# Kernel tuning notes

Hardware: AMD Instinct MI355X
Metric: run time of the kernel (lower is better)

## Reference

```python
import jax, jax.numpy as jnp
import numpy as np

HD = 64        # hidden_dim
H = 4          # heads
N = 50000      # nodes
E = 400000     # edges (before self loops)
NEG_ATT = 0.2  # GATConv attention LeakyReLU slope (PyG default)
NEG_ACT = 0.01 # nn.LeakyReLU() default slope
EPS = 1e-5     # BatchNorm eps


def _bn(x, gamma, beta):
    # training-mode BatchNorm1d over node dimension (biased variance)
    mu = x.mean(0)
    var = x.var(0)
    return gamma * (x - mu) * jax.lax.rsqrt(var + EPS) + beta


def _gatconv(h_in, src, dst, W, a_src, a_dst, bias, heads, outc, concat):
    n = h_in.shape[0]
    h = (h_in @ W.T).reshape(n, heads, outc)              # [N,H,C]
    al_s = jnp.einsum('nhc,hc->nh', h, a_src)             # [N,H]
    al_d = jnp.einsum('nhc,hc->nh', h, a_dst)
    e = jax.nn.leaky_relu(al_s[src] + al_d[dst], NEG_ATT) # [E',H]
    # softmax over incoming edges of each destination node
    m = jax.lax.stop_gradient(jax.ops.segment_max(e, dst, num_segments=n))
    ex = jnp.exp(e - m[dst])
    den = jax.ops.segment_sum(ex, dst, num_segments=n)
    alpha = ex / den[dst]                                  # [E',H]
    out = jax.ops.segment_sum(h[src] * alpha[..., None], dst, num_segments=n)
    out = out.reshape(n, heads * outc) if concat else out.mean(axis=1)
    return out + bias


def setup_inputs() -> dict:
    ks = jax.random.split(jax.random.key(0), 20)
    s = 0.1
    d = {
        'x': jax.random.normal(ks[0], (N, 2 * HD), jnp.float32),
        'edge_index': jax.random.randint(ks[1], (2, E), 0, N, jnp.int64),
        'W1': jax.random.normal(ks[2], (H * HD, 2 * HD), jnp.float32) * s,
        'a1s': jax.random.normal(ks[3], (H, HD), jnp.float32) * s,
        'a1d': jax.random.normal(ks[4], (H, HD), jnp.float32) * s,
        'b1': jnp.zeros((H * HD,), jnp.float32),
        'W2': jax.random.normal(ks[5], (H * HD, H * HD), jnp.float32) * s,
        'a2s': jax.random.normal(ks[6], (H, HD), jnp.float32) * s,
        'a2d': jax.random.normal(ks[7], (H, HD), jnp.float32) * s,
        'b2': jnp.zeros((H * HD,), jnp.float32),
        'W3': jax.random.normal(ks[8], (1 * HD, H * HD), jnp.float32) * s,
        'a3s': jax.random.normal(ks[9], (1, HD), jnp.float32) * s,
        'a3d': jax.random.normal(ks[10], (1, HD), jnp.float32) * s,
        'b3': jnp.zeros((HD,), jnp.float32),
        'gamma': jnp.ones((H * HD,), jnp.float32),
        'beta': jnp.zeros((H * HD,), jnp.float32),
    }
    return d


def reference(x, edge_index, W1, a1s, a1d, b1, W2, a2s, a2d, b2,
              W3, a3s, a3d, b3, gamma, beta):
    n = x.shape[0]
    loop = jnp.arange(n, dtype=edge_index.dtype)
    src = jnp.concatenate([edge_index[0], loop])  # add_self_loops=True
    dst = jnp.concatenate([edge_index[1], loop])

    h = _gatconv(x, src, dst, W1, a1s, a1d, b1, H, HD, True)
    h = jax.nn.leaky_relu(_bn(h, gamma, beta), NEG_ACT)

    # single middle residual block (num_layers=3); dropout is identity (eval)
    res = h
    h = _gatconv(h, src, dst, W2, a2s, a2d, b2, H, HD, True)
    h = jax.nn.leaky_relu(_bn(h, gamma, beta), NEG_ACT)
    h = h + res

    out = _gatconv(h, src, dst, W3, a3s, a3d, b3, 1, HD, False)
    return out
```

## Files before the change

kernel.cpp:

```cpp
#include <hip/hip_runtime.h>
#include <hip/hip_bf16.h>

#define NEG_ATT 0.2f
#define NEG_ACT 0.01f
#define LOG2E 1.4426950408889634f

typedef __attribute__((ext_vector_type(8))) short short8;
typedef __attribute__((ext_vector_type(4))) float f32x4;

__device__ __forceinline__ float b2f(unsigned short h) {
    return __uint_as_float((unsigned int)h << 16);
}
__device__ __forceinline__ unsigned cvt_pk_bf16(float lo, float hi) {
    unsigned r;
    asm("v_cvt_pk_bf16_f32 %0, %1, %2" : "=v"(r) : "v"(lo), "v"(hi));
    return r;
}
__device__ __forceinline__ float fexp2(float x) {
#if __has_builtin(__builtin_amdgcn_exp2f)
    return __builtin_amdgcn_exp2f(x);
#else
    return exp2f(x);
#endif
}


#define SCAN_CHUNK 1024
__global__ void scan1(const int* __restrict__ deg, int* __restrict__ offs,
                      int* blocksum, int Nn) {
    __shared__ int sh[256];
    int b = blockIdx.x, t = threadIdx.x;
    int base = b * SCAN_CHUNK + t * 4;
    int v[4];
    int s = 0;
    for (int j = 0; j < 4; j++) {
        int idx = base + j;
        v[j] = (idx < Nn) ? deg[idx] + 1 : 0;
        s += v[j];
    }
    sh[t] = s;
    __syncthreads();
    for (int off = 1; off < 256; off <<= 1) {
        int x = (t >= off) ? sh[t - off] : 0;
        __syncthreads();
        sh[t] += x;
        __syncthreads();
    }
    int excl = sh[t] - s;
    if (t == 255) blocksum[b] = sh[255];
    int run = excl;
    for (int j = 0; j < 4; j++) {
        int idx = base + j;
        if (idx < Nn) offs[idx] = run;
        run += v[j];
    }
}

__global__ void scan23(int* __restrict__ offs, const int* __restrict__ bsum,
                       int* __restrict__ cursor, int Nn, int G) {
    int i = blockIdx.x * 256 + threadIdx.x;
    if (i > Nn) return;
    int g = i >> 10;
    int basev = 0;
    for (int k = 0; k < g; k++) basev += bsum[k];
    if (i == Nn) {
        int tot = basev;
        for (int k = g; k < G; k++) tot += bsum[k];
        offs[Nn] = tot;
        return;
    }
    int v = offs[i] + basev;
    offs[i] = v;
    cursor[i] = v;
}

__global__ void fill_csr(const int* __restrict__ ei, int* cursor, int* csr, int E, int Nn) {
    int t = blockIdx.x * 256 + threadIdx.x;
    if (t < E) {
        int s = ei[t];
        int d = ei[E + t];
        int p = atomicAdd(&cursor[d], 1);
        csr[p] = s;
    } else if (t < E + Nn) {
        int nn = t - E;
        int p = atomicAdd(&cursor[nn], 1);
        csr[p] = nn;
    }
}


__global__ __launch_bounds__(256) void prep_all(
    int* __restrict__ deg, const int* __restrict__ ei, int E,
    const float* __restrict__ x, unsigned short* __restrict__ xb, int nx, int nxpad,
    const float* __restrict__ w1, unsigned short* __restrict__ o1, int n1,
    const float* __restrict__ w2, unsigned short* __restrict__ o2, int n2,
    const float* __restrict__ w3, unsigned short* __restrict__ o3, int n3) {
    int id = blockIdx.x * 256 + threadIdx.x;
    int nconv = (nxpad + n1 + n2 + n3) / 8;
    if (id >= nconv) {
        int e = id - nconv;
        if (e < E) atomicAdd(&deg[ei[E + e]], 1);
        return;
    }
    int i = id * 8;
    const float* in;
    unsigned short* out;
    if (i < nxpad) {
        if (i >= nx) {
            *(ushort4*)&xb[i] = make_ushort4(0, 0, 0, 0);
            *(ushort4*)&xb[i + 4] = make_ushort4(0, 0, 0, 0);
            return;
        }
        in = x + i; out = xb + i;
    } else {
        int j = i - nxpad;
        if (j < n1) { in = w1 + j; out = o1 + j; }
        else if (j < n1 + n2) { in = w2 + (j - n1); out = o2 + (j - n1); }
        else { in = w3 + (j - n1 - n2); out = o3 + (j - n1 - n2); }
    }
    float4 a = *(const float4*)in;
    float4 b = *(const float4*)(in + 4);
    uint4 o;
    o.x = cvt_pk_bf16(a.x, a.y);
    o.y = cvt_pk_bf16(a.z, a.w);
    o.z = cvt_pk_bf16(b.x, b.y);
    o.w = cvt_pk_bf16(b.z, b.w);
    *(uint4*)out = o;
}

template <bool RES>
__device__ __forceinline__ unsigned bnpack2(unsigned short ya, unsigned short yb_,
                                            float sca, float scb, float sha, float shb,
                                            unsigned short ra, unsigned short rb_) {
    float v0 = sca * b2f(ya) + sha; v0 = v0 > 0.f ? v0 : NEG_ACT * v0;
    float v1 = scb * b2f(yb_) + shb; v1 = v1 > 0.f ? v1 : NEG_ACT * v1;
    if (RES) { v0 += b2f(ra); v1 += b2f(rb_); }
    return cvt_pk_bf16(v0, v1);
}


template <int K, int CO, int HEADS, bool FUSE, bool FRES, bool FWOUT>
__global__ __launch_bounds__(256) void gemm_mfma(
    const unsigned short* __restrict__ Xb, const unsigned short* __restrict__ Wb,
    unsigned short* __restrict__ Hb, const float* __restrict__ a_s,
    const float* __restrict__ a_d, float* __restrict__ als, float* __restrict__ ald,
    const unsigned short* __restrict__ Yb_in, unsigned short* __restrict__ RWbuf,
    const float* __restrict__ scale, const float* __restrict__ shift, int Nn) {
    constexpr int BM = 128, BK = 64, LD = 72, SLD = 68;
    __shared__ __align__(16) char smem[4 * 32 * SLD * 4];
    unsigned short* As = (unsigned short*)smem;
    unsigned short* Bs = As + BM * LD;
    int tid = threadIdx.x;
    int wave = tid >> 6, lane = tid & 63;
    int quad = lane >> 4, l16 = lane & 15;
    int mt, hd;
    if (HEADS == 4) {
        int gm = gridDim.x >> 2;
        int gm8 = gm & ~7;
        int nfull = gm8 * 4;
        int id = blockIdx.x;
        if (id < nfull) {
            int r = id & 31;
            mt = (id >> 5) * 8 + (r & 7);
            hd = r >> 3;
        } else {
            int t2 = id - nfull;
            mt = gm8 + (t2 >> 2);
            hd = t2 & 3;
        }
    } else {
        mt = blockIdx.x;
        hd = 0;
    }
    int m0 = mt * BM, n0 = hd * 64;
    int arow = tid >> 3;
    int achk = (tid & 7) * 8;
    f32x4 acc[2][4] = {};
    for (int k0 = 0; k0 < K; k0 += BK) {
        __syncthreads();
        if (FUSE) {
            int cb = k0 + achk;
            float4 sc0 = *(const float4*)&scale[cb];
            float4 sc1 = *(const float4*)&scale[cb + 4];
            float4 sh0 = *(const float4*)&shift[cb];
            float4 sh1 = *(const float4*)&shift[cb + 4];
#pragma unroll
            for (int p = 0; p < 4; p++) {
                int r = arow + p * 32;
                int m = m0 + r;
                uint4 o = make_uint4(0, 0, 0, 0);
                if (m < Nn) {
                    ushort4 ua = *(const ushort4*)&Yb_in[(size_t)m * 256 + cb];
                    ushort4 ub = *(const ushort4*)&Yb_in[(size_t)m * 256 + cb + 4];
                    ushort4 ra = make_ushort4(0, 0, 0, 0), rb = ra;
                    if (FRES) {
                        ra = *(const ushort4*)&RWbuf[(size_t)m * 256 + cb];
                        rb = *(const ushort4*)&RWbuf[(size_t)m * 256 + cb + 4];
                    }
                    o.x = bnpack2<FRES>(ua.x, ua.y, sc0.x, sc0.y, sh0.x, sh0.y, ra.x, ra.y);
                    o.y = bnpack2<FRES>(ua.z, ua.w, sc0.z, sc0.w, sh0.z, sh0.w, ra.z, ra.w);
                    o.z = bnpack2<FRES>(ub.x, ub.y, sc1.x, sc1.y, sh1.x, sh1.y, rb.x, rb.y);
                    o.w = bnpack2<FRES>(ub.z, ub.w, sc1.z, sc1.w, sh1.z, sh1.w, rb.z, rb.w);
                    if (FWOUT && hd == 0)
                        *(uint4*)&RWbuf[(size_t)m * 256 + cb] = o;
                }
                *(uint4*)&As[r * LD + achk] = o;
            }
        } else {
#pragma unroll
            for (int p = 0; p < 4; p++) {
                int r = arow + p * 32;
                *(int4*)&As[r * LD + achk] = *(const int4*)&Xb[(size_t)(m0 + r) * K + k0 + achk];
            }
        }
#pragma unroll
        for (int p = 0; p < 2; p++) {
            int r = arow + p * 32;
            *(int4*)&Bs[r * LD + achk] = *(const int4*)&Wb[(size_t)(n0 + r) * K + k0 + achk];
        }
        __syncthreads();
#pragma unroll
        for (int ks = 0; ks < 2; ks++) {
            short8 af[2], bfr[4];
#pragma unroll
            for (int i = 0; i < 2; i++)
                af[i] = *(const short8*)&As[(wave * 32 + i * 16 + l16) * LD + ks * 32 + quad * 8];
#pragma unroll
            for (int j = 0; j < 4; j++)
                bfr[j] = *(const short8*)&Bs[(j * 16 + l16) * LD + ks * 32 + quad * 8];
#pragma unroll
            for (int i = 0; i < 2; i++)
#pragma unroll
                for (int j = 0; j < 4; j++)
                    acc[i][j] = __builtin_amdgcn_mfma_f32_16x16x32_bf16(af[i], bfr[j], acc[i][j], 0, 0, 0);
        }
    }
    __syncthreads();

    float asv[4], adv[4];
#pragma unroll
    for (int j = 0; j < 4; j++) {
        asv[j] = a_s[hd * 64 + j * 16 + l16] * LOG2E;
        adv[j] = a_d[hd * 64 + j * 16 + l16] * LOG2E;
    }
#pragma unroll
    for (int i = 0; i < 2; i++)
#pragma unroll
        for (int r = 0; r < 4; r++) {
            float ps = acc[i][0][r] * asv[0] + acc[i][1][r] * asv[1] +
                       acc[i][2][r] * asv[2] + acc[i][3][r] * asv[3];
            float pd = acc[i][0][r] * adv[0] + acc[i][1][r] * adv[1] +
                       acc[i][2][r] * adv[2] + acc[i][3][r] * adv[3];
#pragma unroll
            for (int mm = 1; mm < 16; mm <<= 1) {
                ps += __shfl_xor(ps, mm);
                pd += __shfl_xor(pd, mm);
            }
            if (l16 == 0) {
                int m = m0 + wave * 32 + i * 16 + quad * 4 + r;
                als[m * HEADS + hd] = ps;
                ald[m * HEADS + hd] = pd;
            }
        }

    float* stg = (float*)smem + wave * 32 * SLD;
#pragma unroll
    for (int i = 0; i < 2; i++)
#pragma unroll
        for (int j = 0; j < 4; j++)
#pragma unroll
            for (int r = 0; r < 4; r++)
                stg[(i * 16 + quad * 4 + r) * SLD + j * 16 + l16] = acc[i][j][r];
    int g = lane >> 3, c8 = (lane & 7) * 8;
#pragma unroll
    for (int p = 0; p < 4; p++) {
        int row = p * 8 + g;
        float4 v0 = *(const float4*)&stg[row * SLD + c8];
        float4 v1 = *(const float4*)&stg[row * SLD + c8 + 4];
        uint4 o;
        o.x = cvt_pk_bf16(v0.x, v0.y);
        o.y = cvt_pk_bf16(v0.z, v0.w);
        o.z = cvt_pk_bf16(v1.x, v1.y);
        o.w = cvt_pk_bf16(v1.z, v1.w);
        *(uint4*)&Hb[(size_t)(m0 + wave * 32 + row) * CO + n0 + c8] = o;
    }
}


#define EDGE4(J)                                                                     \
    {                                                                                \
        int s0 = __builtin_amdgcn_readlane(idx, (J));                                \
        int s1 = __builtin_amdgcn_readlane(idx, (J) + 1);                            \
        int s2 = __builtin_amdgcn_readlane(idx, (J) + 2);                            \
        int s3 = __builtin_amdgcn_readlane(idx, (J) + 3);                            \
        const unsigned short* r0 = Hb + (size_t)s0 * 256;                            \
        const unsigned short* r1 = Hb + (size_t)s1 * 256;                            \
        const unsigned short* r2 = Hb + (size_t)s2 * 256;                            \
        const unsigned short* r3 = Hb + (size_t)s3 * 256;                            \
        float a0 = als[s0 * 4 + hd], a1 = als[s1 * 4 + hd];                          \
        float a2 = als[s2 * 4 + hd], a3 = als[s3 * 4 + hd];                          \
        ushort4 h0 = *(const ushort4*)&r0[c4];                                       \
        ushort4 h1 = *(const ushort4*)&r1[c4];                                       \
        ushort4 h2 = *(const ushort4*)&r2[c4];                                       \
        ushort4 h3 = *(const ushort4*)&r3[c4];                                       \
        float e0 = a0 + aldn; e0 = fmaxf(e0, NEG_ATT * e0);                          \
        float e1 = a1 + aldn; e1 = fmaxf(e1, NEG_ATT * e1);                          \
        float e2 = a2 + aldn; e2 = fmaxf(e2, NEG_ATT * e2);                          \
        float e3 = a3 + aldn; e3 = fmaxf(e3, NEG_ATT * e3);                          \
        float w0 = fexp2(e0), w1 = fexp2(e1), w2 = fexp2(e2), w3 = fexp2(e3);        \
        den += (w0 + w1) + (w2 + w3);                                                \
        acc.x += w0 * b2f(h0.x) + w1 * b2f(h1.x) + w2 * b2f(h2.x) + w3 * b2f(h3.x);  \
        acc.y += w0 * b2f(h0.y) + w1 * b2f(h1.y) + w2 * b2f(h2.y) + w3 * b2f(h3.y);  \
        acc.z += w0 * b2f(h0.z) + w1 * b2f(h1.z) + w2 * b2f(h2.z) + w3 * b2f(h3.z);  \
        acc.w += w0 * b2f(h0.w) + w1 * b2f(h1.w) + w2 * b2f(h2.w) + w3 * b2f(h3.w);  \
    }

__global__ __launch_bounds__(256) void aggregate_h4(
    const unsigned short* __restrict__ Hb, const float* __restrict__ als,
    const float* __restrict__ ald, const int* __restrict__ offs,
    const int* __restrict__ csr, unsigned short* __restrict__ Yb, int Nn) {
    int wave = threadIdx.x >> 6;
    int lane = threadIdx.x & 63;
    int n = blockIdx.x * 4 + wave;
    if (n >= Nn) return;
    int hd = lane >> 4;
    int c4 = lane * 4;
    float aldn = ald[n * 4 + hd];
    int beg = __builtin_amdgcn_readfirstlane(offs[n]);
    int end = __builtin_amdgcn_readfirstlane(offs[n + 1]);
    float4 acc = make_float4(0.f, 0.f, 0.f, 0.f);
    float den = 0.f;
    for (int b = beg; b < end; b += 64) {
        int cnt = min(64, end - b);
        int idx = 0;
        if (lane < cnt) idx = csr[b + lane];
        int j = 0;
        for (; j + 8 <= cnt; j += 8) {
            EDGE4(j);
            EDGE4(j + 4);
        }
        for (; j + 4 <= cnt; j += 4) {
            EDGE4(j);
        }
        for (; j < cnt; j++) {
            int s = __builtin_amdgcn_readlane(idx, j);
            const unsigned short* rr = Hb + (size_t)s * 256;
            float e = als[s * 4 + hd] + aldn;
            e = fmaxf(e, NEG_ATT * e);
            float w = fexp2(e);
            den += w;
            ushort4 hv = *(const ushort4*)&rr[c4];
            acc.x += w * b2f(hv.x); acc.y += w * b2f(hv.y);
            acc.z += w * b2f(hv.z); acc.w += w * b2f(hv.w);
        }
    }
    float inv = 1.f / den;
    uint2 o;
    o.x = cvt_pk_bf16(acc.x * inv, acc.y * inv);
    o.y = cvt_pk_bf16(acc.z * inv, acc.w * inv);
    *(uint2*)&Yb[(size_t)n * 256 + c4] = o;
}

__global__ __launch_bounds__(256) void aggregate_h1(
    const unsigned short* __restrict__ Hb, const float* __restrict__ als,
    const float* __restrict__ ald, const int* __restrict__ offs,
    const int* __restrict__ csr, const float* __restrict__ bias,
    float* __restrict__ Yout, int Nn) {
    int wave = threadIdx.x >> 6;
    int lane = threadIdx.x & 63;
    int sub = lane >> 4, lane16 = lane & 15;
    int n = blockIdx.x * 16 + wave * 4 + sub;
    if (n >= Nn) return;
    int c4 = lane16 * 4;
    float aldn = ald[n];
    int beg = offs[n], end = offs[n + 1];
    float4 acc = make_float4(0.f, 0.f, 0.f, 0.f);
    float den = 0.f;
    for (int b = beg; b < end; b += 16) {
        int cnt = min(16, end - b);
        int idx = 0;
        if (lane16 < cnt) idx = csr[b + lane16];
        int j = 0;
        for (; j + 4 <= cnt; j += 4) {
            int s0 = __shfl(idx, (sub << 4) + j);
            int s1 = __shfl(idx, (sub << 4) + j + 1);
            int s2 = __shfl(idx, (sub << 4) + j + 2);
            int s3 = __shfl(idx, (sub << 4) + j + 3);
            float a0 = als[s0], a1 = als[s1], a2 = als[s2], a3 = als[s3];
            ushort4 h0 = *(const ushort4*)&Hb[(size_t)s0 * 64 + c4];
            ushort4 h1 = *(const ushort4*)&Hb[(size_t)s1 * 64 + c4];
            ushort4 h2 = *(const ushort4*)&Hb[(size_t)s2 * 64 + c4];
            ushort4 h3 = *(const ushort4*)&Hb[(size_t)s3 * 64 + c4];
            float e0 = a0 + aldn; e0 = fmaxf(e0, NEG_ATT * e0);
            float e1 = a1 + aldn; e1 = fmaxf(e1, NEG_ATT * e1);
            float e2 = a2 + aldn; e2 = fmaxf(e2, NEG_ATT * e2);
            float e3 = a3 + aldn; e3 = fmaxf(e3, NEG_ATT * e3);
            float w0 = fexp2(e0), w1 = fexp2(e1), w2 = fexp2(e2), w3 = fexp2(e3);
            den += (w0 + w1) + (w2 + w3);
            acc.x += w0 * b2f(h0.x) + w1 * b2f(h1.x) + w2 * b2f(h2.x) + w3 * b2f(h3.x);
            acc.y += w0 * b2f(h0.y) + w1 * b2f(h1.y) + w2 * b2f(h2.y) + w3 * b2f(h3.y);
            acc.z += w0 * b2f(h0.z) + w1 * b2f(h1.z) + w2 * b2f(h2.z) + w3 * b2f(h3.z);
            acc.w += w0 * b2f(h0.w) + w1 * b2f(h1.w) + w2 * b2f(h2.w) + w3 * b2f(h3.w);
        }
        for (; j < cnt; j++) {
            int s = __shfl(idx, (sub << 4) + j);
            float e = als[s] + aldn;
            e = fmaxf(e, NEG_ATT * e);
            float w = fexp2(e);
            den += w;
            ushort4 hv = *(const ushort4*)&Hb[(size_t)s * 64 + c4];
            acc.x += w * b2f(hv.x); acc.y += w * b2f(hv.y);
            acc.z += w * b2f(hv.z); acc.w += w * b2f(hv.w);
        }
    }
    float inv = 1.f / den;
    float4 bv = *(const float4*)&bias[c4];
    float4 o = make_float4(acc.x * inv + bv.x, acc.y * inv + bv.y,
                           acc.z * inv + bv.z, acc.w * inv + bv.w);
    *(float4*)&Yout[(size_t)n * 64 + c4] = o;
}


__global__ __launch_bounds__(256) void bn_stats(const unsigned short* __restrict__ Yb,
                                                float* __restrict__ partial, int Nn) {
    __shared__ float red[4 * 512];
    int t = threadIdx.x;
    int g = blockIdx.x;
    int rows_per = (Nn + gridDim.x - 1) / gridDim.x;
    int r0 = g * rows_per;
    int r1 = min(r0 + rows_per, Nn);
    int sub = t >> 6;
    int c4 = (t & 63) * 4;
    float4 s = make_float4(0.f, 0.f, 0.f, 0.f);
    float4 q = make_float4(0.f, 0.f, 0.f, 0.f);
    for (int r = r0 + sub; r < r1; r += 4) {
        ushort4 u = *(const ushort4*)&Yb[(size_t)r * 256 + c4];
        float vx = b2f(u.x), vy = b2f(u.y), vz = b2f(u.z), vw = b2f(u.w);
        s.x += vx; s.y += vy; s.z += vz; s.w += vw;
        q.x += vx * vx; q.y += vy * vy; q.z += vz * vz; q.w += vw * vw;
    }
    float* rs = &red[sub * 512];
    rs[c4 + 0] = s.x; rs[c4 + 1] = s.y; rs[c4 + 2] = s.z; rs[c4 + 3] = s.w;
    rs[256 + c4 + 0] = q.x; rs[256 + c4 + 1] = q.y;
    rs[256 + c4 + 2] = q.z; rs[256 + c4 + 3] = q.w;
    __syncthreads();
    float v0 = red[t] + red[512 + t] + red[1024 + t] + red[1536 + t];
    float v1 = red[256 + t] + red[768 + t] + red[1280 + t] + red[1792 + t];
    partial[(size_t)g * 512 + t] = v0;
    partial[(size_t)g * 512 + 256 + t] = v1;
}

__global__ __launch_bounds__(256) void bn_reduce_final(
    const float* __restrict__ partial, int NP, const float* __restrict__ gamma,
    const float* __restrict__ beta, float* scale, float* shift, int Nn) {
    __shared__ float sh[8];
    int ch = blockIdx.x;
    int t = threadIdx.x;
    int wave = t >> 6, lane = t & 63;
    float s = 0.f, q = 0.f;
    for (int i = t; i < NP; i += 256) {
        s += partial[(size_t)i * 512 + ch];
        q += partial[(size_t)i * 512 + 256 + ch];
    }
    for (int off = 32; off; off >>= 1) {
        s += __shfl_down(s, off);
        q += __shfl_down(q, off);
    }
    if (lane == 0) { sh[wave] = s; sh[4 + wave] = q; }
    __syncthreads();
    if (t == 0) {
        s = sh[0] + sh[1] + sh[2] + sh[3];
        q = sh[4] + sh[5] + sh[6] + sh[7];
        float inv_n = 1.f / (float)Nn;
        float mu = s * inv_n;
        float var = q * inv_n - mu * mu;
        float sc = gamma[ch] * rsqrtf(var + 1e-5f);
        scale[ch] = sc;
        shift[ch] = beta[ch] - mu * sc;
    }
}


extern "C" void kernel_launch(void* const* d_in, const int* in_sizes, int n_in,
                              void* d_out, int out_size, void* d_ws, size_t ws_size,
                              hipStream_t stream) {
    const float* x    = (const float*)d_in[0];
    const int*   ei   = (const int*)d_in[1];
    const float* W1   = (const float*)d_in[2];
    const float* a1s  = (const float*)d_in[3];
    const float* a1d  = (const float*)d_in[4];
    const float* W2   = (const float*)d_in[6];
    const float* a2s  = (const float*)d_in[7];
    const float* a2d  = (const float*)d_in[8];
    const float* W3   = (const float*)d_in[10];
    const float* a3s  = (const float*)d_in[11];
    const float* a3d  = (const float*)d_in[12];
    const float* b3   = (const float*)d_in[13];
    const float* gamma = (const float*)d_in[14];
    const float* beta  = (const float*)d_in[15];
    float* out = (float*)d_out;

    const int Nn = in_sizes[0] / 128;
    const int E  = in_sizes[1] / 2;
    const int Ep = E + Nn;
    const int Mpad = (Nn + 127) & ~127;

    size_t off = 0;
    char* base = (char*)d_ws;
    auto alloc = [&](size_t bytes) -> void* {
        void* p = base + off;
        off = (off + bytes + 255) & ~(size_t)255;
        return p;
    };
    unsigned short* Hb   = (unsigned short*)alloc((size_t)Mpad * 256 * 2);
    unsigned short* Yb   = (unsigned short*)alloc((size_t)Nn * 256 * 2);
    unsigned short* xb1  = (unsigned short*)alloc((size_t)Mpad * 128 * 2);
    unsigned short* xbig = (unsigned short*)alloc((size_t)Mpad * 256 * 2);
    unsigned short* wb1  = (unsigned short*)alloc((size_t)256 * 128 * 2);
    unsigned short* wb2  = (unsigned short*)alloc((size_t)256 * 256 * 2);
    unsigned short* wb3  = (unsigned short*)alloc((size_t)64 * 256 * 2);
    float* als    = (float*)alloc((size_t)Mpad * 4 * 4);
    float* ald    = (float*)alloc((size_t)Mpad * 4 * 4);
    int*   deg    = (int*)alloc((size_t)Nn * 4);
    int*   offs   = (int*)alloc((size_t)(Nn + 1) * 4);
    int*   cursor = (int*)alloc((size_t)Nn * 4);
    int*   bsum   = (int*)alloc(64 * 4);
    int*   csr    = (int*)alloc((size_t)Ep * 4);
    const int NP = 1024;
    float* partial = (float*)alloc((size_t)NP * 512 * 4);
    float* scale  = (float*)alloc(256 * 4);
    float* shift  = (float*)alloc(256 * 4);
    (void)ws_size;

    const int G = (Nn + SCAN_CHUNK - 1) / SCAN_CHUNK;

    hipMemsetAsync(deg, 0, (size_t)Nn * 4, stream);
    {
        int nxpad = Mpad * 128;
        int wtot = 256 * 128 + 256 * 256 + 64 * 256;
        int nconv = (nxpad + wtot) / 8;
        prep_all<<<(nconv + E + 255) / 256, 256, 0, stream>>>(
            deg, ei, E, x, xb1, Nn * 128, nxpad,
            W1, wb1, 256 * 128, W2, wb2, 256 * 256, W3, wb3, 64 * 256);
    }

    scan1<<<G, 256, 0, stream>>>(deg, offs, bsum, Nn);
    scan23<<<(Nn + 1 + 255) / 256, 256, 0, stream>>>(offs, bsum, cursor, Nn, G);
    fill_csr<<<(Ep + 255) / 256, 256, 0, stream>>>(ei, cursor, csr, E, Nn);

    const int gm = Mpad / 128;
    const int nagg4 = (Nn + 3) / 4;
    const int nagg1 = (Nn + 15) / 16;

    gemm_mfma<128, 256, 4, false, false, false><<<gm * 4, 256, 0, stream>>>(
        xb1, wb1, Hb, a1s, a1d, als, ald, nullptr, nullptr, nullptr, nullptr, 0);
    aggregate_h4<<<nagg4, 256, 0, stream>>>(Hb, als, ald, offs, csr, Yb, Nn);
    bn_stats<<<NP, 256, 0, stream>>>(Yb, partial, Nn);
    bn_reduce_final<<<256, 256, 0, stream>>>(partial, NP, gamma, beta, scale, shift, Nn);

    gemm_mfma<256, 256, 4, true, false, true><<<gm * 4, 256, 0, stream>>>(
        nullptr, wb2, Hb, a2s, a2d, als, ald, Yb, xbig, scale, shift, Nn);
    aggregate_h4<<<nagg4, 256, 0, stream>>>(Hb, als, ald, offs, csr, Yb, Nn);
    bn_stats<<<NP, 256, 0, stream>>>(Yb, partial, Nn);
    bn_reduce_final<<<256, 256, 0, stream>>>(partial, NP, gamma, beta, scale, shift, Nn);

    gemm_mfma<256, 64, 1, true, true, false><<<gm, 256, 0, stream>>>(
        nullptr, wb3, Hb, a3s, a3d, als, ald, Yb, xbig, scale, shift, Nn);
    aggregate_h1<<<nagg1, 256, 0, stream>>>(Hb, als, ald, offs, csr, b3, out, Nn);
}
```

Baseline: 325.1 us.

## Fuse BN stats with final reduce and recompute residual instead of storing it

Merges the BN partial-stats and final-reduce kernels into one launch. The last block to finish, detected by an atomic counter, computes scale and shift, and the partial-block count drops from 1024 to 512. The separate residual write (xbig) from the layer-2 GEMM is removed; the layer-3 GEMM instead recomputes the layer-1 BN+LeakyReLU from a kept copy of Yb1 using the saved scale0/shift0. This saves two kernel launches and a residual buffer write, at the cost of an extra Yb buffer, extra arithmetic in the layer-3 GEMM, and a serial reduction by one block.

```diff
diff --git a/kernel.cpp b/kernel.cpp
--- a/kernel.cpp
+++ b/kernel.cpp
@@ -4,6 +4,7 @@
 #define NEG_ATT 0.2f
 #define NEG_ACT 0.01f
 #define LOG2E 1.4426950408889634f
+#define NPBN 512
 
 typedef __attribute__((ext_vector_type(8))) short short8;
 typedef __attribute__((ext_vector_type(4))) float f32x4;
@@ -131,21 +132,27 @@
 template <bool RES>
 __device__ __forceinline__ unsigned bnpack2(unsigned short ya, unsigned short yb_,
                                             float sca, float scb, float sha, float shb,
-                                            unsigned short ra, unsigned short rb_) {
-    float v0 = sca * b2f(ya) + sha; v0 = v0 > 0.f ? v0 : NEG_ACT * v0;
-    float v1 = scb * b2f(yb_) + shb; v1 = v1 > 0.f ? v1 : NEG_ACT * v1;
-    if (RES) { v0 += b2f(ra); v1 += b2f(rb_); }
+                                            unsigned short ra, unsigned short rb_,
+                                            float rca, float rcb, float rha, float rhb) {
+    float v0 = sca * b2f(ya) + sha; v0 = fmaxf(v0, NEG_ACT * v0);
+    float v1 = scb * b2f(yb_) + shb; v1 = fmaxf(v1, NEG_ACT * v1);
+    if (RES) {
+        float r0 = rca * b2f(ra) + rha; r0 = fmaxf(r0, NEG_ACT * r0);
+        float r1 = rcb * b2f(rb_) + rhb; r1 = fmaxf(r1, NEG_ACT * r1);
+        v0 += r0; v1 += r1;
+    }
     return cvt_pk_bf16(v0, v1);
 }
 
 
-template <int K, int CO, int HEADS, bool FUSE, bool FRES, bool FWOUT>
+template <int K, int CO, int HEADS, bool FUSE, bool FRES>
 __global__ __launch_bounds__(256) void gemm_mfma(
     const unsigned short* __restrict__ Xb, const unsigned short* __restrict__ Wb,
     unsigned short* __restrict__ Hb, const float* __restrict__ a_s,
     const float* __restrict__ a_d, float* __restrict__ als, float* __restrict__ ald,
-    const unsigned short* __restrict__ Yb_in, unsigned short* __restrict__ RWbuf,
-    const float* __restrict__ scale, const float* __restrict__ shift, int Nn) {
+    const unsigned short* __restrict__ Yb_in, const unsigned short* __restrict__ RWbuf,
+    const float* __restrict__ scale, const float* __restrict__ shift,
+    const float* __restrict__ scale_r, const float* __restrict__ shift_r, int Nn) {
     constexpr int BM = 128, BK = 64, LD = 72, SLD = 68;
     __shared__ __align__(16) char smem[4 * 32 * SLD * 4];
     unsigned short* As = (unsigned short*)smem;
@@ -184,6 +191,13 @@
             float4 sc1 = *(const float4*)&scale[cb + 4];
             float4 sh0 = *(const float4*)&shift[cb];
             float4 sh1 = *(const float4*)&shift[cb + 4];
+            float4 rc0 = make_float4(0, 0, 0, 0), rc1 = rc0, rh0 = rc0, rh1 = rc0;
+            if (FRES) {
+                rc0 = *(const float4*)&scale_r[cb];
+                rc1 = *(const float4*)&scale_r[cb + 4];
+                rh0 = *(const float4*)&shift_r[cb];
+                rh1 = *(const float4*)&shift_r[cb + 4];
+            }
 #pragma unroll
             for (int p = 0; p < 4; p++) {
                 int r = arow + p * 32;
@@ -197,12 +211,14 @@
                         ra = *(const ushort4*)&RWbuf[(size_t)m * 256 + cb];
                         rb = *(const ushort4*)&RWbuf[(size_t)m * 256 + cb + 4];
                     }
-                    o.x = bnpack2<FRES>(ua.x, ua.y, sc0.x, sc0.y, sh0.x, sh0.y, ra.x, ra.y);
-                    o.y = bnpack2<FRES>(ua.z, ua.w, sc0.z, sc0.w, sh0.z, sh0.w, ra.z, ra.w);
-                    o.z = bnpack2<FRES>(ub.x, ub.y, sc1.x, sc1.y, sh1.x, sh1.y, rb.x, rb.y);
-                    o.w = bnpack2<FRES>(ub.z, ub.w, sc1.z, sc1.w, sh1.z, sh1.w, rb.z, rb.w);
-                    if (FWOUT && hd == 0)
-                        *(uint4*)&RWbuf[(size_t)m * 256 + cb] = o;
+                    o.x = bnpack2<FRES>(ua.x, ua.y, sc0.x, sc0.y, sh0.x, sh0.y,
+                                        ra.x, ra.y, rc0.x, rc0.y, rh0.x, rh0.y);
+                    o.y = bnpack2<FRES>(ua.z, ua.w, sc0.z, sc0.w, sh0.z, sh0.w,
+                                        ra.z, ra.w, rc0.z, rc0.w, rh0.z, rh0.w);
+                    o.z = bnpack2<FRES>(ub.x, ub.y, sc1.x, sc1.y, sh1.x, sh1.y,
+                                        rb.x, rb.y, rc1.x, rc1.y, rh1.x, rh1.y);
+                    o.w = bnpack2<FRES>(ub.z, ub.w, sc1.z, sc1.w, sh1.z, sh1.w,
+                                        rb.z, rb.w, rc1.z, rc1.w, rh1.z, rh1.w);
                 }
                 *(uint4*)&As[r * LD + achk] = o;
             }
@@ -421,12 +437,17 @@
 }
 
 
-__global__ __launch_bounds__(256) void bn_stats(const unsigned short* __restrict__ Yb,
-                                                float* __restrict__ partial, int Nn) {
+__global__ __launch_bounds__(256) void bn_stats_final(
+    const unsigned short* __restrict__ Yb, float* __restrict__ partial,
+    int* __restrict__ cnt, const float* __restrict__ gamma,
+    const float* __restrict__ beta, float* __restrict__ scale,
+    float* __restrict__ shift, int Nn) {
     __shared__ float red[4 * 512];
+    __shared__ int isLast;
     int t = threadIdx.x;
     int g = blockIdx.x;
-    int rows_per = (Nn + gridDim.x - 1) / gridDim.x;
+    int NP = gridDim.x;
+    int rows_per = (Nn + NP - 1) / NP;
     int r0 = g * rows_per;
     int r1 = min(r0 + rows_per, Nn);
     int sub = t >> 6;
@@ -446,38 +467,32 @@
     __syncthreads();
     float v0 = red[t] + red[512 + t] + red[1024 + t] + red[1536 + t];
     float v1 = red[256 + t] + red[768 + t] + red[1280 + t] + red[1792 + t];
-    partial[(size_t)g * 512 + t] = v0;
-    partial[(size_t)g * 512 + 256 + t] = v1;
-}
-
-__global__ __launch_bounds__(256) void bn_reduce_final(
-    const float* __restrict__ partial, int NP, const float* __restrict__ gamma,
-    const float* __restrict__ beta, float* scale, float* shift, int Nn) {
-    __shared__ float sh[8];
-    int ch = blockIdx.x;
-    int t = threadIdx.x;
-    int wave = t >> 6, lane = t & 63;
-    float s = 0.f, q = 0.f;
-    for (int i = t; i < NP; i += 256) {
-        s += partial[(size_t)i * 512 + ch];
-        q += partial[(size_t)i * 512 + 256 + ch];
-    }
-    for (int off = 32; off; off >>= 1) {
-        s += __shfl_down(s, off);
-        q += __shfl_down(q, off);
-    }
-    if (lane == 0) { sh[wave] = s; sh[4 + wave] = q; }
+    __hip_atomic_store(&partial[(size_t)g * 512 + t], v0,
+                       __ATOMIC_RELAXED, __HIP_MEMORY_SCOPE_AGENT);
+    __hip_atomic_store(&partial[(size_t)g * 512 + 256 + t], v1,
+                       __ATOMIC_RELAXED, __HIP_MEMORY_SCOPE_AGENT);
+    __threadfence();
     __syncthreads();
     if (t == 0) {
-        s = sh[0] + sh[1] + sh[2] + sh[3];
-        q = sh[4] + sh[5] + sh[6] + sh[7];
-        float inv_n = 1.f / (float)Nn;
-        float mu = s * inv_n;
-        float var = q * inv_n - mu * mu;
-        float sc = gamma[ch] * rsqrtf(var + 1e-5f);
-        scale[ch] = sc;
-        shift[ch] = beta[ch] - mu * sc;
-    }
+        int old = atomicAdd(cnt, 1);
+        isLast = (old == NP - 1);
+    }
+    __syncthreads();
+    if (!isLast) return;
+    float ssum = 0.f, qsum = 0.f;
+#pragma unroll 8
+    for (int i = 0; i < NP; i++) {
+        ssum += __hip_atomic_load(&partial[(size_t)i * 512 + t],
+                                  __ATOMIC_RELAXED, __HIP_MEMORY_SCOPE_AGENT);
+        qsum += __hip_atomic_load(&partial[(size_t)i * 512 + 256 + t],
+                                  __ATOMIC_RELAXED, __HIP_MEMORY_SCOPE_AGENT);
+    }
+    float inv_n = 1.f / (float)Nn;
+    float mu = ssum * inv_n;
+    float var = qsum * inv_n - mu * mu;
+    float sc = gamma[t] * rsqrtf(var + 1e-5f);
+    scale[t] = sc;
+    shift[t] = beta[t] - mu * sc;
 }
 
 
@@ -513,28 +528,32 @@
         return p;
     };
     unsigned short* Hb   = (unsigned short*)alloc((size_t)Mpad * 256 * 2);
-    unsigned short* Yb   = (unsigned short*)alloc((size_t)Nn * 256 * 2);
+    unsigned short* Yb1  = (unsigned short*)alloc((size_t)Nn * 256 * 2);
+    unsigned short* Yb2  = (unsigned short*)alloc((size_t)Nn * 256 * 2);
     unsigned short* xb1  = (unsigned short*)alloc((size_t)Mpad * 128 * 2);
-    unsigned short* xbig = (unsigned short*)alloc((size_t)Mpad * 256 * 2);
     unsigned short* wb1  = (unsigned short*)alloc((size_t)256 * 128 * 2);
     unsigned short* wb2  = (unsigned short*)alloc((size_t)256 * 256 * 2);
     unsigned short* wb3  = (unsigned short*)alloc((size_t)64 * 256 * 2);
     float* als    = (float*)alloc((size_t)Mpad * 4 * 4);
     float* ald    = (float*)alloc((size_t)Mpad * 4 * 4);
+    size_t zoff0 = off;
     int*   deg    = (int*)alloc((size_t)Nn * 4);
+    int*   cnts   = (int*)alloc(2 * 4);
+    size_t zbytes = off - zoff0;
     int*   offs   = (int*)alloc((size_t)(Nn + 1) * 4);
     int*   cursor = (int*)alloc((size_t)Nn * 4);
     int*   bsum   = (int*)alloc(64 * 4);
     int*   csr    = (int*)alloc((size_t)Ep * 4);
-    const int NP = 1024;
-    float* partial = (float*)alloc((size_t)NP * 512 * 4);
-    float* scale  = (float*)alloc(256 * 4);
-    float* shift  = (float*)alloc(256 * 4);
+    float* partial = (float*)alloc((size_t)NPBN * 512 * 4);
+    float* scale0 = (float*)alloc(256 * 4);
+    float* shift0 = (float*)alloc(256 * 4);
+    float* scale1 = (float*)alloc(256 * 4);
+    float* shift1 = (float*)alloc(256 * 4);
     (void)ws_size;
 
     const int G = (Nn + SCAN_CHUNK - 1) / SCAN_CHUNK;
 
-    hipMemsetAsync(deg, 0, (size_t)Nn * 4, stream);
+    hipMemsetAsync(deg, 0, zbytes, stream);
     {
         int nxpad = Mpad * 128;
         int wtot = 256 * 128 + 256 * 256 + 64 * 256;
@@ -552,19 +571,22 @@
     const int nagg4 = (Nn + 3) / 4;
     const int nagg1 = (Nn + 15) / 16;
 
-    gemm_mfma<128, 256, 4, false, false, false><<<gm * 4, 256, 0, stream>>>(
-        xb1, wb1, Hb, a1s, a1d, als, ald, nullptr, nullptr, nullptr, nullptr, 0);
-    aggregate_h4<<<nagg4, 256, 0, stream>>>(Hb, als, ald, offs, csr, Yb, Nn);
-    bn_stats<<<NP, 256, 0, stream>>>(Yb, partial, Nn);
-    bn_reduce_final<<<256, 256, 0, stream>>>(partial, NP, gamma, beta, scale, shift, Nn);
-
-    gemm_mfma<256, 256, 4, true, false, true><<<gm * 4, 256, 0, stream>>>(
-        nullptr, wb2, Hb, a2s, a2d, als, ald, Yb, xbig, scale, shift, Nn);
-    aggregate_h4<<<nagg4, 256, 0, stream>>>(Hb, als, ald, offs, csr, Yb, Nn);
-    bn_stats<<<NP, 256, 0, stream>>>(Yb, partial, Nn);
-    bn_reduce_final<<<256, 256, 0, stream>>>(partial, NP, gamma, beta, scale, shift, Nn);
-
-    gemm_mfma<256, 64, 1, true, true, false><<<gm, 256, 0, stream>>>(
-        nullptr, wb3, Hb, a3s, a3d, als, ald, Yb, xbig, scale, shift, Nn);
+    gemm_mfma<128, 256, 4, false, false><<<gm * 4, 256, 0, stream>>>(
+        xb1, wb1, Hb, a1s, a1d, als, ald, nullptr, nullptr,
+        nullptr, nullptr, nullptr, nullptr, Nn);
+    aggregate_h4<<<nagg4, 256, 0, stream>>>(Hb, als, ald, offs, csr, Yb1, Nn);
+    bn_stats_final<<<NPBN, 256, 0, stream>>>(Yb1, partial, cnts, gamma, beta,
+                                             scale0, shift0, Nn);
+
+    gemm_mfma<256, 256, 4, true, false><<<gm * 4, 256, 0, stream>>>(
+        nullptr, wb2, Hb, a2s, a2d, als, ald, Yb1, nullptr,
+        scale0, shift0, nullptr, nullptr, Nn);
+    aggregate_h4<<<nagg4, 256, 0, stream>>>(Hb, als, ald, offs, csr, Yb2, Nn);
+    bn_stats_final<<<NPBN, 256, 0, stream>>>(Yb2, partial, cnts + 1, gamma, beta,
+                                             scale1, shift1, Nn);
+
+    gemm_mfma<256, 64, 1, true, true><<<gm, 256, 0, stream>>>(
+        nullptr, wb3, Hb, a3s, a3d, als, ald, Yb2, Yb1,
+        scale1, shift1, scale0, shift0, Nn);
     aggregate_h1<<<nagg1, 256, 0, stream>>>(Hb, als, ald, offs, csr, b3, out, Nn);
 }
```

After: 427.6 us. 31.5% more time.
